# Optimization experiments

Measured on AMD Instinct MI355X. Metric: run time of the kernel, lower is better.

## Reference

```python
import jax, jax.numpy as jnp
import numpy as np

B, N, D, H, K, MSL = 16, 512, 512, 8, 16, 512
HD = D // H
EPS = 1e-5


def _ln(x, g, b):
    m = jnp.mean(x, axis=-1, keepdims=True)
    v = jnp.mean((x - m) ** 2, axis=-1, keepdims=True)
    return (x - m) * jax.lax.rsqrt(v + EPS) * g + b


def setup_inputs() -> dict:
    key = jax.random.key(0)
    ks = jax.random.split(key, 12)
    s = 0.02
    d = {
        'x': jax.random.normal(ks[0], (B, N, D), jnp.float32),
        'wq': jax.random.normal(ks[1], (D, D), jnp.float32) * s,
        'bq': jnp.zeros((D,), jnp.float32),
        'wk': jax.random.normal(ks[2], (D, D), jnp.float32) * s,
        'bk': jnp.zeros((D,), jnp.float32),
        'wv': jax.random.normal(ks[3], (D, D), jnp.float32) * s,
        'bv': jnp.zeros((D,), jnp.float32),
        'wo': jax.random.normal(ks[4], (D, D), jnp.float32) * s,
        'bo': jnp.zeros((D,), jnp.float32),
        'g1': jnp.ones((D,), jnp.float32),
        'be1': jnp.zeros((D,), jnp.float32),
        'g2': jnp.ones((D,), jnp.float32),
        'be2': jnp.zeros((D,), jnp.float32),
        'w1': jax.random.normal(ks[5], (D, 4 * D), jnp.float32) * s,
        'bf1': jnp.zeros((4 * D,), jnp.float32),
        'w2': jax.random.normal(ks[6], (4 * D, D), jnp.float32) * s,
        'bf2': jnp.zeros((D,), jnp.float32),
        'rel_emb': jax.random.normal(ks[7], (2 * MSL - 1, H), jnp.float32) * s,
    }
    return d


def reference(x, wq, bq, wk, bk, wv, bv, wo, bo, g1, be1, g2, be2, w1, bf1, w2, bf2, rel_emb):
    # Pre-norm attention (dropout = identity, eval mode)
    xn = _ln(x, g1, be1)
    Q = (xn @ wq + bq).reshape(B, N, H, HD)
    Kh = (xn @ wk + bk).reshape(B, N, H, HD)
    V = (xn @ wv + bv).reshape(B, N, H, HD)
    scale = HD ** -0.5
    logits = jnp.einsum('bnhd,bmhd->bhnm', Q, Kh) * scale  # (B,H,N,N)
    # relative temporal bias
    pos = jnp.arange(N)
    drel = pos[None, :] - pos[:, None] + (MSL - 1)  # (N,N)
    bias = rel_emb[drel]  # (N,N,H)
    logits = logits + jnp.transpose(bias, (2, 0, 1))[None]
    # top-k sparsification + softmax over surviving entries only
    vals, idx = jax.lax.top_k(logits, K)  # (B,H,N,K)
    attn_k = jax.nn.softmax(vals, axis=-1)  # softmax over -inf-masked row == softmax over top-k
    # scatter probabilities back into dense (B,H,N,N) rows
    rows = jnp.zeros((B * H * N, N), logits.dtype)
    attn = jax.vmap(lambda r, i, v: r.at[i].set(v))(
        rows, idx.reshape(-1, K), attn_k.reshape(-1, K)
    ).reshape(B, H, N, N)
    out = jnp.einsum('bhnm,bmhd->bnhd', attn, V).reshape(B, N, D)
    out = out @ wo + bo
    x = x + out
    # feed-forward (GELU exact, matching torch default)
    xn2 = _ln(x, g2, be2)
    ff = jax.nn.gelu(xn2 @ w1 + bf1, approximate=False) @ w2 + bf2
    return x + ff
```

## Files before the change

### kernel.cpp

```cpp
#include <hip/hip_runtime.h>
#include <hip/hip_bf16.h>

#define BB 16
#define NN 512
#define DD 512
#define HH 8
#define HD 64
#define MM (BB*NN)
#define DFF 2048

typedef __attribute__((ext_vector_type(8))) short bf16x8;
typedef __attribute__((ext_vector_type(4))) float fx4;

static __device__ __forceinline__ unsigned short f2bf(float f) {
  unsigned u = __float_as_uint(f);
  u += 0x7FFFu + ((u >> 16) & 1u);
  return (unsigned short)(u >> 16);
}
static __device__ __forceinline__ float bf2f(unsigned short s) {
  return __uint_as_float(((unsigned)s) << 16);
}

static __device__ __forceinline__ void load_lds16(const unsigned short* g, unsigned short* l) {
  __builtin_amdgcn_global_load_lds(
      (const __attribute__((address_space(1))) void*)g,
      (__attribute__((address_space(3))) void*)l, 16, 0, 0);
}

__global__ void transpose_all(const float* __restrict__ wq, const float* __restrict__ wk,
                              const float* __restrict__ wv, const float* __restrict__ wo,
                              const float* __restrict__ w1, const float* __restrict__ w2,
                              unsigned short* __restrict__ wqkvT, unsigned short* __restrict__ woT,
                              unsigned short* __restrict__ w1T, unsigned short* __restrict__ w2T) {
  __shared__ float tl[32][33];
  int id = blockIdx.x;
  const float* src; unsigned short* dst; int K, N, bx, by;
  if (id < 1024) {
    int m = id >> 8, tt = id & 255;
    src = (m == 0) ? wq : (m == 1) ? wk : (m == 2) ? wv : wo;
    dst = (m == 3) ? woT : wqkvT + m * 512 * 512;
    K = 512; N = 512; bx = tt & 15; by = tt >> 4;
  } else if (id < 2048) {
    int tt = id - 1024;
    src = w1; dst = w1T; K = 512; N = 2048; bx = tt & 63; by = tt >> 6;
  } else {
    int tt = id - 2048;
    src = w2; dst = w2T; K = 2048; N = 512; bx = tt & 15; by = tt >> 4;
  }
  int tx = threadIdx.x, ty = threadIdx.y;
  int x0 = bx * 32, y0 = by * 32;
  #pragma unroll
  for (int i = 0; i < 4; i++)
    tl[ty + i*8][tx] = src[(size_t)(y0 + ty + i*8) * N + x0 + tx];
  __syncthreads();
  #pragma unroll
  for (int i = 0; i < 4; i++)
    dst[(size_t)(x0 + ty + i*8) * K + y0 + tx] = f2bf(tl[tx][ty + i*8]);
}

__global__ void concat_bias(const float* __restrict__ bq, const float* __restrict__ bk,
                            const float* __restrict__ bv, float* __restrict__ o) {
  int t = blockIdx.x * 256 + threadIdx.x;
  if (t < 512) o[t] = bq[t];
  else if (t < 1024) o[t] = bk[t - 512];
  else if (t < 1536) o[t] = bv[t - 1024];
}

__global__ __launch_bounds__(256) void ln_kernel(const float* __restrict__ X,
                                                 const float* __restrict__ g,
                                                 const float* __restrict__ be,
                                                 unsigned short* __restrict__ O) {
  int w = threadIdx.x >> 6, l = threadIdx.x & 63;
  size_t row = (size_t)blockIdx.x * 4 + w;
  const float* xr = X + row * 512;
  fx4 a = *(const fx4*)(xr + l*4);
  fx4 c = *(const fx4*)(xr + 256 + l*4);
  float s = a[0]+a[1]+a[2]+a[3] + c[0]+c[1]+c[2]+c[3];
  float q = a[0]*a[0]+a[1]*a[1]+a[2]*a[2]+a[3]*a[3]
          + c[0]*c[0]+c[1]*c[1]+c[2]*c[2]+c[3]*c[3];
  #pragma unroll
  for (int s2 = 1; s2 < 64; s2 <<= 1) { s += __shfl_xor(s, s2); q += __shfl_xor(q, s2); }
  float mean = s * (1.0f/512.0f);
  float var  = q * (1.0f/512.0f) - mean*mean;
  float rs = rsqrtf(var + 1e-5f);
  fx4 ga = *(const fx4*)(g + l*4);
  fx4 gc = *(const fx4*)(g + 256 + l*4);
  fx4 ba = *(const fx4*)(be + l*4);
  fx4 bc = *(const fx4*)(be + 256 + l*4);
  ushort4 o1, o2;
  o1.x = f2bf((a[0]-mean)*rs*ga[0] + ba[0]);
  o1.y = f2bf((a[1]-mean)*rs*ga[1] + ba[1]);
  o1.z = f2bf((a[2]-mean)*rs*ga[2] + ba[2]);
  o1.w = f2bf((a[3]-mean)*rs*ga[3] + ba[3]);
  o2.x = f2bf((c[0]-mean)*rs*gc[0] + bc[0]);
  o2.y = f2bf((c[1]-mean)*rs*gc[1] + bc[1]);
  o2.z = f2bf((c[2]-mean)*rs*gc[2] + bc[2]);
  o2.w = f2bf((c[3]-mean)*rs*gc[3] + bc[3]);
  *(ushort4*)(O + row*512 + l*4) = o1;
  *(ushort4*)(O + row*512 + 256 + l*4) = o2;
}

template<int MODE, int TN>
__global__ __launch_bounds__(256) void gemm_kernel(
    const unsigned short* __restrict__ A,
    const unsigned short* __restrict__ Bm,
    const float* __restrict__ bias,
    const float* resid,
    void* C,
    int M, int N, int K) {
  constexpr int MI  = (TN == 128) ? 2 : 1;
  constexpr int BW  = (TN == 128) ? 32 : 16;
  constexpr int NBI = (TN == 128) ? 4 : 2;
  __shared__ unsigned short As[64*64];
  __shared__ unsigned short Bs[TN*64];
  int m0 = blockIdx.y * 64, n0 = blockIdx.x * TN;
  int t = threadIdx.x;
  int w = t >> 6, l = t & 63;
  int wm = (TN == 128) ? (w >> 1) : w;
  int wn = (TN == 128) ? (w & 1) : 0;
  int lid = l & 15, quad = l >> 4;
  int lrow = l >> 3, lch = (l & 7) ^ lrow;

  const unsigned short* gA = A  + (size_t)(m0 + w*16 + lrow)*K + lch*8;
  const unsigned short* gB = Bm + (size_t)(n0 + w*BW + lrow)*K + lch*8;
  unsigned short* lA0 = As + (w*16    )*64;
  unsigned short* lA1 = As + (w*16 + 8)*64;
  unsigned short* lB[NBI];
  #pragma unroll
  for (int i = 0; i < NBI; i++) lB[i] = Bs + (w*BW + i*8)*64;

  fx4 acc[MI][4];
  #pragma unroll
  for (int i = 0; i < MI; i++)
    #pragma unroll
    for (int j = 0; j < 4; j++) acc[i][j] = (fx4){0.f,0.f,0.f,0.f};

  int xA = (lid & 7) * 8;

  for (int k0 = 0; k0 < K; k0 += 64) {
    load_lds16(gA,       lA0);
    load_lds16(gA + 8*K, lA1);
    #pragma unroll
    for (int i = 0; i < NBI; i++) load_lds16(gB + (size_t)(i*8)*K, lB[i]);
    gA += 64; gB += 64;
    __syncthreads();
    #pragma unroll
    for (int s = 0; s < 2; s++) {
      int cbase = (s*4 + quad) * 8;
      bf16x8 af[MI], bf[4];
      #pragma unroll
      for (int i = 0; i < MI; i++) {
        int ra = wm*(MI*16) + i*16 + lid;
        af[i] = *(const bf16x8*)(As + ra*64 + (cbase ^ xA));
      }
      #pragma unroll
      for (int j = 0; j < 4; j++) {
        int rb = wn*64 + j*16 + lid;
        bf[j] = *(const bf16x8*)(Bs + rb*64 + (cbase ^ xA));
      }
      #pragma unroll
      for (int i = 0; i < MI; i++)
        #pragma unroll
        for (int j = 0; j < 4; j++)
          acc[i][j] = __builtin_amdgcn_mfma_f32_16x16x32_bf16(af[i], bf[j], acc[i][j], 0, 0, 0);
    }
    __syncthreads();
  }

  #pragma unroll
  for (int i = 0; i < MI; i++) {
    #pragma unroll
    for (int j = 0; j < 4; j++) {
      int col = n0 + wn*64 + j*16 + lid;
      float bv = bias[col];
      #pragma unroll
      for (int r = 0; r < 4; r++) {
        int row = m0 + wm*(MI*16) + i*16 + quad*4 + r;
        float v = acc[i][j][r] + bv;
        if (MODE == 0) {
          if (col < 512) v *= 0.125f;
          ((unsigned short*)C)[(size_t)row*N + col] = f2bf(v);
        } else if (MODE == 1 || MODE == 3) {
          v += resid[(size_t)row*N + col];
          ((float*)C)[(size_t)row*N + col] = v;
        } else {
          float gl = 0.5f * v * (1.0f + erff(v * 0.70710678118654752f));
          ((unsigned short*)C)[(size_t)row*N + col] = f2bf(gl);
        }
      }
    }
  }
}

__global__ __launch_bounds__(256) void attn_kernel(
    const unsigned short* __restrict__ QKV,
    const float* __restrict__ rel_emb,
    unsigned short* __restrict__ Aout) {
  __shared__ float smem[10752];
  unsigned short* Ks = (unsigned short*)smem;
  float* bias_s = smem + 9216;
  float* pr = smem + 10240;
  int blk = blockIdx.x;
  int q0 = (blk & 7) << 6;
  int bh = blk >> 3;
  int b = bh >> 3, h = bh & 7;
  int t = threadIdx.x;
  int w = t >> 6, l = t & 63;
  int lid = l & 15, quad = l >> 4;

  for (int i = t; i < 1023; i += 256) bias_s[i] = rel_emb[i*8 + h];

  int qn = q0 + w*16 + lid;
  const unsigned short* qp = QKV + ((size_t)(b*512 + qn))*1536 + h*64 + quad*8;
  bf16x8 qf0 = *(const bf16x8*)qp;
  bf16x8 qf1 = *(const bf16x8*)(qp + 32);

  fx4 acc[32];
  #pragma unroll
  for (int i = 0; i < 32; i++) acc[i] = (fx4){0.f,0.f,0.f,0.f};

  #pragma unroll
  for (int half = 0; half < 2; half++) {
    __syncthreads();
    #pragma unroll
    for (int i = 0; i < 8; i++) {
      int c = t + i*256;
      int row = c >> 3, ch = c & 7;
      uint4 d = *(const uint4*)(QKV + ((size_t)(b*512 + half*256 + row))*1536 + 512 + h*64 + ch*8);
      *(uint4*)(Ks + row*72 + ch*8) = d;
    }
    __syncthreads();
    #pragma unroll
    for (int kt = 0; kt < 16; kt++) {
      const unsigned short* kp = Ks + (kt*16 + lid)*72 + quad*8;
      bf16x8 kb0 = *(const bf16x8*)kp;
      bf16x8 kb1 = *(const bf16x8*)(kp + 32);
      int ai = half*16 + kt;
      acc[ai] = __builtin_amdgcn_mfma_f32_16x16x32_bf16(qf0, kb0, acc[ai], 0, 0, 0);
      acc[ai] = __builtin_amdgcn_mfma_f32_16x16x32_bf16(qf1, kb1, acc[ai], 0, 0, 0);
    }
  }

  int nb = q0 + w*16 + quad*4;
  #pragma unroll
  for (int kt = 0; kt < 32; kt++) {
    int m = kt*16 + lid;
    int bidx = m - nb + 511;
    #pragma unroll
    for (int r = 0; r < 4; r++) {
      float v = acc[kt][r] + bias_s[bidx - r];
      unsigned mu = __float_as_uint(v);
      mu = (mu & 0x80000000u) ? ~mu : (mu | 0x80000000u);
      acc[kt][r] = __uint_as_float((mu & 0xFFFFFE00u) | (unsigned)(511 - m));
    }
  }

  unsigned lo0=0, lo1=0, lo2=0, lo3=0;
  unsigned hi0=0xFFFFFFFFu, hi1=0xFFFFFFFFu, hi2=0xFFFFFFFFu, hi3=0xFFFFFFFFu;
  unsigned th0=0, th1=0, th2=0, th3=0;
  unsigned done = 0;
  #pragma unroll 1
  for (int it = 0; it < 34; ++it) {
    unsigned d_;
    d_ = hi0-lo0; unsigned mid0 = lo0 + (d_>>1) + (d_&1u);
    d_ = hi1-lo1; unsigned mid1 = lo1 + (d_>>1) + (d_&1u);
    d_ = hi2-lo2; unsigned mid2 = lo2 + (d_>>1) + (d_&1u);
    d_ = hi3-lo3; unsigned mid3 = lo3 + (d_>>1) + (d_&1u);
    unsigned c0=0, c1=0, c2=0, c3=0;
    #pragma unroll
    for (int kt = 0; kt < 32; kt++) {
      c0 += (__float_as_uint(acc[kt][0]) >= mid0);
      c1 += (__float_as_uint(acc[kt][1]) >= mid1);
      c2 += (__float_as_uint(acc[kt][2]) >= mid2);
      c3 += (__float_as_uint(acc[kt][3]) >= mid3);
    }
    unsigned p01 = c0 | (c1 << 16);
    unsigned p23 = c2 | (c3 << 16);
    #pragma unroll
    for (int s2 = 1; s2 < 16; s2 <<= 1) {
      p01 += __shfl_xor(p01, s2);
      p23 += __shfl_xor(p23, s2);
    }
    unsigned C0 = p01 & 0xFFFFu, C1 = p01 >> 16;
    unsigned C2 = p23 & 0xFFFFu, C3 = p23 >> 16;
    { bool f = !(done & 1u); bool e = f && (C0 == 16u);
      th0 = e ? mid0 : th0; done |= e ? 1u : 0u;
      lo0 = (f && C0 > 16u) ? mid0 : lo0; hi0 = (f && C0 < 16u) ? mid0 : hi0; }
    { bool f = !(done & 2u); bool e = f && (C1 == 16u);
      th1 = e ? mid1 : th1; done |= e ? 2u : 0u;
      lo1 = (f && C1 > 16u) ? mid1 : lo1; hi1 = (f && C1 < 16u) ? mid1 : hi1; }
    { bool f = !(done & 4u); bool e = f && (C2 == 16u);
      th2 = e ? mid2 : th2; done |= e ? 4u : 0u;
      lo2 = (f && C2 > 16u) ? mid2 : lo2; hi2 = (f && C2 < 16u) ? mid2 : hi2; }
    { bool f = !(done & 8u); bool e = f && (C3 == 16u);
      th3 = e ? mid3 : th3; done |= e ? 8u : 0u;
      lo3 = (f && C3 > 16u) ? mid3 : lo3; hi3 = (f && C3 < 16u) ? mid3 : hi3; }
    if (__all((int)(done == 15u))) break;
  }

  float* prE = pr + w*128 + quad*32;
  int*   prM = (int*)prE + 16;
  unsigned below = (1u << lid) - 1u;
  #pragma unroll
  for (int r = 0; r < 4; r++) {
    unsigned thr = (r==0) ? th0 : (r==1) ? th1 : (r==2) ? th2 : th3;
    int base = 0;
    #pragma unroll
    for (int kt = 0; kt < 32; kt++) {
      unsigned u = __float_as_uint(acc[kt][r]);
      bool sel = u >= thr;
      unsigned long long bm = __ballot(sel);
      unsigned gm = (unsigned)(bm >> (quad*16)) & 0xFFFFu;
      if (sel) {
        int slot = base + __popc(gm & below);
        unsigned vu = u & 0xFFFFFE00u;
        vu = (vu & 0x80000000u) ? (vu & 0x7FFFFFFFu) : ~vu;
        float e = exp2f(__uint_as_float(vu) * 1.44269504f);
        if (slot < 16) { prE[slot] = e; prM[slot] = 511 - (int)(u & 0x1FFu); }
      }
      base += __popc(gm);
    }
    __threadfence_block();
    int n = nb + r;
    float o0=0.f, o1=0.f, o2=0.f, o3=0.f, es=0.f;
    #pragma unroll
    for (int k2 = 0; k2 < 16; k2++) {
      float e = prE[k2];
      int m = prM[k2];
      const unsigned short* vp = QKV + ((size_t)(b*512 + m))*1536 + 1024 + h*64 + lid*4;
      ushort4 v4 = *(const ushort4*)vp;
      es += e;
      o0 += e * bf2f(v4.x); o1 += e * bf2f(v4.y);
      o2 += e * bf2f(v4.z); o3 += e * bf2f(v4.w);
    }
    float inv = 1.0f / es;
    ushort4 ov;
    ov.x = f2bf(o0*inv); ov.y = f2bf(o1*inv);
    ov.z = f2bf(o2*inv); ov.w = f2bf(o3*inv);
    *(ushort4*)(Aout + ((size_t)(b*512 + n))*512 + h*64 + lid*4) = ov;
    __threadfence_block();
  }
}

extern "C" void kernel_launch(void* const* d_in, const int* in_sizes, int n_in,
                              void* d_out, int out_size, void* d_ws, size_t ws_size,
                              hipStream_t stream) {
  const float* x   = (const float*)d_in[0];
  const float* wq  = (const float*)d_in[1];
  const float* bq  = (const float*)d_in[2];
  const float* wk  = (const float*)d_in[3];
  const float* bk  = (const float*)d_in[4];
  const float* wv  = (const float*)d_in[5];
  const float* bv  = (const float*)d_in[6];
  const float* wo  = (const float*)d_in[7];
  const float* bo  = (const float*)d_in[8];
  const float* g1  = (const float*)d_in[9];
  const float* be1 = (const float*)d_in[10];
  const float* g2  = (const float*)d_in[11];
  const float* be2 = (const float*)d_in[12];
  const float* w1  = (const float*)d_in[13];
  const float* bf1 = (const float*)d_in[14];
  const float* w2  = (const float*)d_in[15];
  const float* bf2 = (const float*)d_in[16];
  const float* rel = (const float*)d_in[17];

  char* p = (char*)d_ws;
  size_t off = 0;
  auto alloc = [&](size_t bytes) {
    size_t cur = off;
    off += (bytes + 255) & ~(size_t)255;
    return (void*)(p + cur);
  };
  unsigned short* wqkvT = (unsigned short*)alloc((size_t)1536*512*2);
  unsigned short* woT   = (unsigned short*)alloc((size_t)512*512*2);
  unsigned short* w1T   = (unsigned short*)alloc((size_t)2048*512*2);
  unsigned short* w2T   = (unsigned short*)alloc((size_t)512*2048*2);
  float*          bqkv  = (float*)alloc(1536*4);
  unsigned short* R1    = (unsigned short*)alloc((size_t)MM*512*2);
  unsigned short* R2    = (unsigned short*)alloc((size_t)MM*2048*2);

  unsigned short* xn1  = R1;
  unsigned short* aout = R1;
  unsigned short* xn2  = R1;
  unsigned short* qkvb = R2;
  unsigned short* hbuf = R2;
  float*          x2   = (float*)d_out;
  (void)ws_size; (void)in_sizes; (void)n_in; (void)out_size;

  transpose_all<<<3072, dim3(32, 8), 0, stream>>>(wq, wk, wv, wo, w1, w2,
                                                  wqkvT, woT, w1T, w2T);
  concat_bias<<<6, 256, 0, stream>>>(bq, bk, bv, bqkv);

  ln_kernel<<<2048, 256, 0, stream>>>(x, g1, be1, xn1);
  gemm_kernel<0,128><<<dim3(12, 128), 256, 0, stream>>>(xn1, wqkvT, bqkv, nullptr, qkvb, MM, 1536, 512);
  attn_kernel<<<1024, 256, 0, stream>>>(qkvb, rel, aout);
  gemm_kernel<1,64><<<dim3(8, 128), 256, 0, stream>>>(aout, woT, bo, x, x2, MM, 512, 512);
  ln_kernel<<<2048, 256, 0, stream>>>(x2, g2, be2, xn2);
  gemm_kernel<2,128><<<dim3(16, 128), 256, 0, stream>>>(xn2, w1T, bf1, nullptr, hbuf, MM, 2048, 512);
  gemm_kernel<3,64><<<dim3(8, 128), 256, 0, stream>>>(hbuf, w2T, bf2, x2, (float*)d_out, MM, 512, 2048);
}
```

Baseline: 411.6 us.

## Shrink key tile LDS and narrow top-k bisection bounds from lane min/max

Measured after the change: 463.4 us. 1.13x slower.

```diff
diff --git a/kernel.cpp b/kernel.cpp
--- a/kernel.cpp
+++ b/kernel.cpp
@@ -196,10 +196,10 @@
     const unsigned short* __restrict__ QKV,
     const float* __restrict__ rel_emb,
     unsigned short* __restrict__ Aout) {
-  __shared__ float smem[10752];
+  __shared__ float smem[6144];
   unsigned short* Ks = (unsigned short*)smem;
-  float* bias_s = smem + 9216;
-  float* pr = smem + 10240;
+  float* bias_s = smem + 4608;
+  float* pr = smem + 5632;
   int blk = blockIdx.x;
   int q0 = (blk & 7) << 6;
   int bh = blk >> 3;
@@ -219,23 +219,23 @@
   #pragma unroll
   for (int i = 0; i < 32; i++) acc[i] = (fx4){0.f,0.f,0.f,0.f};
 
-  #pragma unroll
-  for (int half = 0; half < 2; half++) {
+  #pragma unroll 1
+  for (int chunk = 0; chunk < 4; chunk++) {
     __syncthreads();
     #pragma unroll
-    for (int i = 0; i < 8; i++) {
+    for (int i = 0; i < 4; i++) {
       int c = t + i*256;
       int row = c >> 3, ch = c & 7;
-      uint4 d = *(const uint4*)(QKV + ((size_t)(b*512 + half*256 + row))*1536 + 512 + h*64 + ch*8);
+      uint4 d = *(const uint4*)(QKV + ((size_t)(b*512 + chunk*128 + row))*1536 + 512 + h*64 + ch*8);
       *(uint4*)(Ks + row*72 + ch*8) = d;
     }
     __syncthreads();
     #pragma unroll
-    for (int kt = 0; kt < 16; kt++) {
+    for (int kt = 0; kt < 8; kt++) {
       const unsigned short* kp = Ks + (kt*16 + lid)*72 + quad*8;
       bf16x8 kb0 = *(const bf16x8*)kp;
       bf16x8 kb1 = *(const bf16x8*)(kp + 32);
-      int ai = half*16 + kt;
+      int ai = chunk*8 + kt;
       acc[ai] = __builtin_amdgcn_mfma_f32_16x16x32_bf16(qf0, kb0, acc[ai], 0, 0, 0);
       acc[ai] = __builtin_amdgcn_mfma_f32_16x16x32_bf16(qf1, kb1, acc[ai], 0, 0, 0);
     }
@@ -255,8 +255,32 @@
     }
   }
 
-  unsigned lo0=0, lo1=0, lo2=0, lo3=0;
-  unsigned hi0=0xFFFFFFFFu, hi1=0xFFFFFFFFu, hi2=0xFFFFFFFFu, hi3=0xFFFFFFFFu;
+  unsigned mx0=0, mx1=0, mx2=0, mx3=0;
+  #pragma unroll
+  for (int kt = 0; kt < 32; kt++) {
+    unsigned u0 = __float_as_uint(acc[kt][0]); mx0 = u0 > mx0 ? u0 : mx0;
+    unsigned u1 = __float_as_uint(acc[kt][1]); mx1 = u1 > mx1 ? u1 : mx1;
+    unsigned u2 = __float_as_uint(acc[kt][2]); mx2 = u2 > mx2 ? u2 : mx2;
+    unsigned u3 = __float_as_uint(acc[kt][3]); mx3 = u3 > mx3 ? u3 : mx3;
+  }
+  unsigned mn0=mx0, mn1=mx1, mn2=mx2, mn3=mx3;
+  #pragma unroll
+  for (int s2 = 1; s2 < 16; s2 <<= 1) {
+    unsigned o;
+    o = __shfl_xor(mn0, s2); mn0 = o < mn0 ? o : mn0;
+    o = __shfl_xor(mn1, s2); mn1 = o < mn1 ? o : mn1;
+    o = __shfl_xor(mn2, s2); mn2 = o < mn2 ? o : mn2;
+    o = __shfl_xor(mn3, s2); mn3 = o < mn3 ? o : mn3;
+    o = __shfl_xor(mx0, s2); mx0 = o > mx0 ? o : mx0;
+    o = __shfl_xor(mx1, s2); mx1 = o > mx1 ? o : mx1;
+    o = __shfl_xor(mx2, s2); mx2 = o > mx2 ? o : mx2;
+    o = __shfl_xor(mx3, s2); mx3 = o > mx3 ? o : mx3;
+  }
+  unsigned lo0 = mn0 - (mn0 ? 1u : 0u), hi0 = mx0;
+  unsigned lo1 = mn1 - (mn1 ? 1u : 0u), hi1 = mx1;
+  unsigned lo2 = mn2 - (mn2 ? 1u : 0u), hi2 = mx2;
+  unsigned lo3 = mn3 - (mn3 ? 1u : 0u), hi3 = mx3;
+
   unsigned th0=0, th1=0, th2=0, th3=0;
   unsigned done = 0;
   #pragma unroll 1
```
